# Kernel optimization log

Measured on AMD Instinct MI355X. Metric: run time of the kernel, lower is better.

## Reference

```python
import jax, jax.numpy as jnp
import numpy as np

N = 50000      # nodes
E = 800000     # edges
F_IN = 128     # input features
H = 64         # hidden channels
G = 64         # graphs in batch
EPS = 1e-5


def setup_inputs() -> dict:
    key = jax.random.key(0)
    ks = jax.random.split(key, 24)
    def nrm(k, s):
        return jax.random.normal(k, s, dtype=jnp.float32) * 0.05
    inp = {
        "x": nrm(ks[0], (N, F_IN)),
        "edge_index": jax.random.randint(ks[1], (2, E), 0, N),
        "batch": jnp.sort(jax.random.randint(ks[2], (N,), 0, G)),
        # GCNConv weights (stored [in, out]; math equivalent to torch Linear)
        "W0": nrm(ks[3], (F_IN, H)), "b0": nrm(ks[4], (H,)),
        "W1": nrm(ks[5], (H, H)),    "b1": nrm(ks[6], (H,)),
        "W2": nrm(ks[7], (H, H)),    "b2": nrm(ks[8], (H,)),
        # residual linears
        "RW0": nrm(ks[9], (F_IN, H)),  "rb0": nrm(ks[10], (H,)),
        "RW1": nrm(ks[11], (H, H)),    "rb1": nrm(ks[12], (H,)),
        "RW2": nrm(ks[13], (H, H)),    "rb2": nrm(ks[14], (H,)),
        # layernorm gamma/beta
        "g0": jnp.ones((H,), jnp.float32), "be0": jnp.zeros((H,), jnp.float32),
        "g1": jnp.ones((H,), jnp.float32), "be1": jnp.zeros((H,), jnp.float32),
        "g2": jnp.ones((H,), jnp.float32), "be2": jnp.zeros((H,), jnp.float32),
        # final readout linear
        "lw": nrm(ks[15], (H, 1)), "lb": nrm(ks[16], (1,)),
    }
    return inp


def _layernorm(x, g, b):
    mu = jnp.mean(x, axis=-1, keepdims=True)
    var = jnp.mean(jnp.square(x - mu), axis=-1, keepdims=True)
    return (x - mu) * jax.lax.rsqrt(var + EPS) * g + b


def reference(x, edge_index, batch,
              W0, b0, W1, b1, W2, b2,
              RW0, rb0, RW1, rb1, RW2, rb2,
              g0, be0, g1, be1, g2, be2,
              lw, lb):
    n = x.shape[0]
    loops = jnp.arange(n)
    row = jnp.concatenate([edge_index[0], loops])  # source
    col = jnp.concatenate([edge_index[1], loops])  # target
    # symmetric GCN normalization with self-loops (PyG gcn_norm)
    deg = jax.ops.segment_sum(jnp.ones_like(col, dtype=x.dtype), col, num_segments=n)
    dis = jnp.where(deg > 0, deg ** -0.5, 0.0)
    norm = dis[row] * dis[col]  # [E+N]

    params = [(W0, b0, RW0, rb0, g0, be0),
              (W1, b1, RW1, rb1, g1, be1),
              (W2, b2, RW2, rb2, g2, be2)]
    n_layers = len(params)
    for i, (W, b, RW, rb, g, be) in enumerate(params):
        h = x @ W                                                  # [n, H]
        agg = jax.ops.segment_sum(h[row] * norm[:, None], col, num_segments=n) + b
        x = agg + (x @ RW + rb)                                    # residual
        # dropout: eval mode -> identity
        x = _layernorm(x, g, be)
        if i < n_layers - 1:
            x = jax.nn.relu(x)

    # global mean pool over graphs
    counts = jax.ops.segment_sum(jnp.ones((n,), x.dtype), batch, num_segments=G)
    pooled = jax.ops.segment_sum(x, batch, num_segments=G) / jnp.maximum(counts, 1.0)[:, None]
    return pooled @ lw + lb  # [G, 1]
```

## Files before the change

### kernel.cpp

```cpp
#include <hip/hip_runtime.h>
#include <hip/hip_bf16.h>

#define HID 64
#define NGRAPH 64
#define BSH 7
#define NCH 384

static inline size_t align256(size_t x) { return (x + 255) & ~(size_t)255; }

typedef __attribute__((ext_vector_type(8))) short bf16x8;
typedef __attribute__((ext_vector_type(4))) float f32x4;

__device__ __forceinline__ float ldf(const void* p, size_t i, int f32) {
    if (f32) return ((const float*)p)[i];
    unsigned int w = ((unsigned int)((const unsigned short*)p)[i]) << 16;
    return __uint_as_float(w);
}
__device__ __forceinline__ float bf2f(unsigned short u) {
    return __uint_as_float(((unsigned int)u) << 16);
}
__device__ __forceinline__ unsigned short f2bf(float f) {
    __hip_bfloat16 h = __float2bfloat16(f);
    return *(unsigned short*)&h;
}

__device__ __forceinline__ unsigned char f2e4m3(float f) {
#if defined(__has_builtin) && __has_builtin(__builtin_amdgcn_cvt_pk_fp8_f32)
    int r = __builtin_amdgcn_cvt_pk_fp8_f32(f, f, 0, false);
    return (unsigned char)(r & 0xFF);
#else
    unsigned u = __float_as_uint(f);
    unsigned s = (u >> 24) & 0x80;
    unsigned a = u & 0x7FFFFFFF;
    float af = __uint_as_float(a);
    if (af < 0.015625f) {
        int m = (int)rintf(af * 512.f);
        return (unsigned char)(s | m);
    }
    unsigned r = a + 0x7FFFF + ((a >> 20) & 1);
    int e = (int)(r >> 23) - 127;
    if (e > 8) return (unsigned char)(s | 0x7E);
    return (unsigned char)(s | ((e + 7) << 3) | ((r >> 20) & 7));
#endif
}
template <int IDX>
__device__ __forceinline__ float d8(unsigned p) {
#if defined(__has_builtin) && __has_builtin(__builtin_amdgcn_cvt_f32_fp8)
    return __builtin_amdgcn_cvt_f32_fp8(p, IDX);
#else
    unsigned b = (p >> (IDX * 8)) & 0xFF;
    unsigned e = (b >> 3) & 0xF, m = b & 7;
    float v = e ? __uint_as_float(((e + 120) << 23) | (m << 20))
                : (float)m * (1.f / 512.f);
    return (b & 0x80) ? -v : v;
#endif
}

__global__ void k_sniff(const unsigned short* __restrict__ x, int nwords, int* __restrict__ flag,
                        float* __restrict__ gsum, int* __restrict__ gcnt) {
    __shared__ int cw, cz;
    int t = threadIdx.x;
    if (t == 0) { cw = 0; cz = 0; }
    if (t < NGRAPH) { gsum[t] = 0.f; gcnt[t] = 0; }
    __syncthreads();
    int weird = 0, evenzero = 0;
    for (int i = t; i < nwords; i += blockDim.x) {
        unsigned short u = x[i];
        int e = (u >> 7) & 0xFF;
        if (e >= 128) weird++;
        if (((i & 1) == 0) && ((u & 0x7FFF) == 0)) evenzero++;
    }
    atomicAdd(&cw, weird);
    atomicAdd(&cz, evenzero);
    __syncthreads();
    if (t == 0) *flag = (cw > nwords / 16 || cz > nwords / 8) ? 1 : 0;
}

__global__ __launch_bounds__(256) void k_prep(const int* __restrict__ batch, int* __restrict__ gcnt,
                                              int n, int nbG,
                                              const void* W0, const void* RW0, const void* b0, const void* rb0,
                                              const void* W1, const void* RW1, const void* b1, const void* rb1,
                                              const void* W2, const void* RW2, const void* b2, const void* rb2,
                                              const int* __restrict__ dflag,
                                              unsigned short* wt0, unsigned short* wt1, unsigned short* wt2,
                                              float* bcat,
                                              const int* __restrict__ ecol, int e, int nbuck,
                                              int* __restrict__ hist) {
    __shared__ int sh[1024];
    int b = blockIdx.x, t = threadIdx.x;
    if (b < nbG) {
        if (t < NGRAPH) sh[t] = 0;
        __syncthreads();
        int i = b * 256 + t;
        if (i < n) atomicAdd(&sh[batch[i]], 1);
        __syncthreads();
        if (t < NGRAPH && sh[t] > 0) atomicAdd(&gcnt[t], sh[t]);
    } else if (b < nbG + 130) {
        int f = *dflag;
        int i = (b - nbG) * 256 + t;
        if (i < 16384) {
            int nn = i >> 7, k = i & 127;
            float v = (nn < 64) ? ldf(W0, (size_t)k * 64 + nn, f) : ldf(RW0, (size_t)k * 64 + (nn - 64), f);
            wt0[nn * 128 + k] = f2bf(v);
        } else if (i < 24576) {
            int j = i - 16384; int nn = j >> 6, k = j & 63;
            float v = (nn < 64) ? ldf(W1, (size_t)k * 64 + nn, f) : ldf(RW1, (size_t)k * 64 + (nn - 64), f);
            wt1[nn * 64 + k] = f2bf(v);
        } else if (i < 32768) {
            int j = i - 24576; int nn = j >> 6, k = j & 63;
            float v = (nn < 64) ? ldf(W2, (size_t)k * 64 + nn, f) : ldf(RW2, (size_t)k * 64 + (nn - 64), f);
            wt2[nn * 64 + k] = f2bf(v);
        } else if (i < 32768 + 192) {
            int j = i - 32768; int l = j >> 6, c = j & 63;
            const void* bb = (l == 0) ? b0 : (l == 1) ? b1 : b2;
            const void* rr = (l == 0) ? rb0 : (l == 1) ? rb1 : rb2;
            bcat[l * 64 + c] = ldf(bb, c, f) + ldf(rr, c, f);
        }
    } else {
        int c = b - nbG - 130;
        for (int i = t; i < nbuck; i += 256) sh[i] = 0;
        __syncthreads();
        int per = (e + NCH - 1) / NCH;
        int s = c * per, en = min(e, s + per);
        for (int i = s + t; i < en; i += 256)
            atomicAdd(&sh[ecol[i] >> BSH], 1);
        __syncthreads();
        for (int i = t; i < nbuck; i += 256) hist[i * NCH + c] = sh[i];
    }
}

__global__ void k_scan1(const int* __restrict__ src, int* __restrict__ bsum, int n) {
    __shared__ int s[256];
    int t = threadIdx.x;
    int base = blockIdx.x * 1024 + t * 4;
    int sum = 0;
#pragma unroll
    for (int j = 0; j < 4; j++) { int i = base + j; if (i < n) sum += src[i]; }
    s[t] = sum;
    __syncthreads();
    for (int o = 128; o > 0; o >>= 1) {
        if (t < o) s[t] += s[t + o];
        __syncthreads();
    }
    if (t == 0) bsum[blockIdx.x] = s[0];
}

__global__ void k_scan2(const int* __restrict__ bsum, int* __restrict__ bscan,
                        int* __restrict__ out, int nb, int n) {
    __shared__ int s[256];
    int t = threadIdx.x;
    int v = (t < nb) ? bsum[t] : 0;
    s[t] = v;
    __syncthreads();
    for (int o = 1; o < 256; o <<= 1) {
        int x = (t >= o) ? s[t - o] : 0;
        __syncthreads();
        s[t] += x;
        __syncthreads();
    }
    if (t < nb) bscan[t] = s[t] - v;
    if (t == nb - 1) out[n] = s[t];
}

__global__ void k_scan3(const int* __restrict__ src, const int* __restrict__ bscan,
                        int* __restrict__ out, int n) {
    __shared__ int s[256];
    int t = threadIdx.x;
    int base = blockIdx.x * 1024 + t * 4;
    int tsum = 0;
#pragma unroll
    for (int j = 0; j < 4; j++) { int i = base + j; if (i < n) tsum += src[i]; }
    s[t] = tsum;
    __syncthreads();
    for (int o = 1; o < 256; o <<= 1) {
        int x = (t >= o) ? s[t - o] : 0;
        __syncthreads();
        s[t] += x;
        __syncthreads();
    }
    int off = bscan[blockIdx.x] + s[t] - tsum;
#pragma unroll
    for (int j = 0; j < 4; j++) {
        int i = base + j;
        if (i < n) { out[i] = off; off += src[i]; }
    }
}

__global__ __launch_bounds__(256) void k_scatter(const int* __restrict__ erow,
                                                 const int* __restrict__ ecol, int e, int nbuck,
                                                 const int* __restrict__ hoffs,
                                                 int* __restrict__ esrc,
                                                 unsigned char* __restrict__ et7) {
    __shared__ int cur[1024];
    int c = blockIdx.x, t = threadIdx.x;
    for (int i = t; i < nbuck; i += 256) cur[i] = hoffs[i * NCH + c];
    __syncthreads();
    int per = (e + NCH - 1) / NCH;
    int s = c * per, en = min(e, s + per);
    for (int i = s + t; i < en; i += 256) {
        int tg = ecol[i];
        int p = atomicAdd(&cur[tg >> BSH], 1);
        esrc[p] = erow[i];
        et7[p] = (unsigned char)(tg & 127);
    }
}

__global__ __launch_bounds__(256) void k_bucket(const int* __restrict__ esrc,
                                                const unsigned char* __restrict__ et7,
                                                const int* __restrict__ hoffs,
                                                int nbuck, int n, int e,
                                                int* __restrict__ offs, float* __restrict__ dis,
                                                int* __restrict__ csr) {
    __shared__ int hist[128];
    __shared__ int lofs[128];
    __shared__ int curs[128];
    int b = blockIdx.x, t = threadIdx.x;
    int nb0 = b << BSH;
    int nn = n - nb0; if (nn > 128) nn = 128;
    int s = hoffs[b * NCH];
    int en = (b + 1 < nbuck) ? hoffs[(b + 1) * NCH] : e;
    if (t < 128) hist[t] = 0;
    __syncthreads();
    for (int i = s + t; i < en; i += 256)
        atomicAdd(&hist[et7[i]], 1);
    __syncthreads();
    if (t < 128) lofs[t] = hist[t];
    __syncthreads();
    for (int o = 1; o < 128; o <<= 1) {
        int v = (t < 128 && t >= o) ? lofs[t - o] : 0;
        __syncthreads();
        if (t < 128) lofs[t] += v;
        __syncthreads();
    }
    if (t < nn) {
        int ex = s + lofs[t] - hist[t];
        offs[nb0 + t] = ex;
        curs[t] = ex;
        dis[nb0 + t] = rsqrtf((float)(hist[t] + 1));
    }
    if (b == nbuck - 1 && t == 0) offs[n] = e;
    __syncthreads();
    for (int i = s + t; i < en; i += 256) {
        int p = atomicAdd(&curs[et7[i]], 1);
        csr[p] = esrc[i];
    }
}

template <int K, bool XFLAG, bool LO>
__global__ __launch_bounds__(256) void k_gemm(const void* __restrict__ xin,
                                              const unsigned short* __restrict__ wt,
                                              const float* __restrict__ bcat,
                                              const float* __restrict__ dis,
                                              const int* __restrict__ dflag,
                                              unsigned char* __restrict__ hs,
                                              float* __restrict__ base, int n) {
    const int KP = K + 8;
    __shared__ unsigned short sXh[64 * KP];
    __shared__ unsigned short sXl[LO ? 64 * KP : 1];
    int f32 = *dflag;
    int tid = threadIdx.x;
    int row0 = blockIdx.x * 64;

    if (XFLAG && !f32) {
        const uint4* xv = (const uint4*)xin;
        const int C = K / 8;
        for (int i = tid; i < 64 * C; i += 256) {
            int r = i / C, c = i % C;
            int gr = row0 + r;
            uint4 v = (gr < n) ? xv[(size_t)gr * C + c] : make_uint4(0, 0, 0, 0);
            *(uint4*)&sXh[r * KP + c * 8] = v;
        }
    } else if (XFLAG) {
        for (int i = tid; i < 64 * K; i += 256) {
            int r = i / K, k = i - r * K;
            int gr = row0 + r;
            float v = (gr < n) ? ((const float*)xin)[(size_t)gr * K + k] : 0.f;
            sXh[r * KP + k] = f2bf(v);
        }
    } else {
        const float4* xv = (const float4*)xin;
        const int C = K / 4;
        for (int i = tid; i < 64 * C; i += 256) {
            int r = i / C, c = i % C;
            int gr = row0 + r;
            float4 v = (gr < n) ? xv[(size_t)gr * C + c] : make_float4(0.f, 0.f, 0.f, 0.f);
            ushort4 h, lo;
            h.x = f2bf(v.x); h.y = f2bf(v.y); h.z = f2bf(v.z); h.w = f2bf(v.w);
            if (LO) {
                lo.x = f2bf(v.x - bf2f(h.x)); lo.y = f2bf(v.y - bf2f(h.y));
                lo.z = f2bf(v.z - bf2f(h.z)); lo.w = f2bf(v.w - bf2f(h.w));
            }
            *(ushort4*)&sXh[r * KP + c * 4] = h;
            if (LO) *(ushort4*)&sXl[r * KP + c * 4] = lo;
        }
    }
    __syncthreads();

    int w = tid >> 6, lane = tid & 63;
    int m = lane & 15, q = lane >> 4;
    f32x4 acc[8];
#pragma unroll
    for (int ct = 0; ct < 8; ct++) acc[ct] = (f32x4){0.f, 0.f, 0.f, 0.f};

    int arow = w * 16 + m;
#pragma unroll 1
    for (int ks = 0; ks < K / 32; ks++) {
        int ka = ks * 32 + q * 8;
        bf16x8 ah = *(const bf16x8*)&sXh[arow * KP + ka];
        bf16x8 al;
        if (LO) al = *(const bf16x8*)&sXl[arow * KP + ka];
#pragma unroll
        for (int ct = 0; ct < 8; ct++) {
            bf16x8 bb = *(const bf16x8*)(wt + (size_t)(ct * 16 + m) * K + ka);
            acc[ct] = __builtin_amdgcn_mfma_f32_16x16x32_bf16(ah, bb, acc[ct], 0, 0, 0);
            if (LO) acc[ct] = __builtin_amdgcn_mfma_f32_16x16x32_bf16(al, bb, acc[ct], 0, 0, 0);
        }
    }

#pragma unroll
    for (int ct = 0; ct < 4; ct++) {
        int col = ct * 16 + m;
#pragma unroll
        for (int reg = 0; reg < 4; reg++) {
            int r = row0 + w * 16 + q * 4 + reg;
            if (r < n) {
                float dv = dis[r];
                float h = acc[ct][reg] * dv;
                hs[(size_t)r * 64 + col] = f2e4m3(h);
                base[(size_t)r * 64 + col] = h * dv + acc[ct + 4][reg] + bcat[col];
            }
        }
    }
}

template <bool FINAL>
__global__ __launch_bounds__(1024) void k_agg_ln(const unsigned char* __restrict__ hs,
                                                 const float* __restrict__ base,
                                                 const float* __restrict__ dis,
                                                 const int* __restrict__ offs,
                                                 const int* __restrict__ csr,
                                                 const void* __restrict__ gam,
                                                 const void* __restrict__ bet,
                                                 const int* __restrict__ dflag,
                                                 float* __restrict__ xout, int n, int relu,
                                                 const int* __restrict__ batch,
                                                 const void* __restrict__ lw,
                                                 float* __restrict__ gsum) {
    __shared__ float sG[FINAL ? NGRAPH : 1];
    int f32 = *dflag;
    int t = threadIdx.x;
    if (FINAL) {
        if (t < NGRAPH) sG[t] = 0.f;
        __syncthreads();
    }
    int grp = t >> 4;
    int l = t & 15;
    int gl0 = (t & 63) & ~15;
    int v = blockIdx.x * 64 + grp;
    if (v < n) {
        int s = offs[v];
        int e2 = offs[v + 1];
        float4 bv = *(const float4*)&base[(size_t)v * 64 + l * 4];
        float dv = dis[v];
        float a0 = 0.f, a1 = 0.f, a2 = 0.f, a3 = 0.f;
        int myidx = (s + l < e2) ? csr[s + l] : 0;
        for (int gbase = s; gbase < e2; gbase += 16) {
            int cnt = e2 - gbase; if (cnt > 16) cnt = 16;
            int cur = myidx;
            int nxt = gbase + 16;
            if (nxt < e2) myidx = (nxt + l < e2) ? csr[nxt + l] : 0;
            int j = 0;
            for (; j + 7 < cnt; j += 8) {
                int s0 = __shfl(cur, gl0 + j, 64);
                int s1 = __shfl(cur, gl0 + j + 1, 64);
                int s2 = __shfl(cur, gl0 + j + 2, 64);
                int s3 = __shfl(cur, gl0 + j + 3, 64);
                int s4 = __shfl(cur, gl0 + j + 4, 64);
                int s5 = __shfl(cur, gl0 + j + 5, 64);
                int s6 = __shfl(cur, gl0 + j + 6, 64);
                int s7 = __shfl(cur, gl0 + j + 7, 64);
                unsigned p0 = *(const unsigned*)(hs + (size_t)s0 * 64 + l * 4);
                unsigned p1 = *(const unsigned*)(hs + (size_t)s1 * 64 + l * 4);
                unsigned p2 = *(const unsigned*)(hs + (size_t)s2 * 64 + l * 4);
                unsigned p3 = *(const unsigned*)(hs + (size_t)s3 * 64 + l * 4);
                unsigned p4 = *(const unsigned*)(hs + (size_t)s4 * 64 + l * 4);
                unsigned p5 = *(const unsigned*)(hs + (size_t)s5 * 64 + l * 4);
                unsigned p6 = *(const unsigned*)(hs + (size_t)s6 * 64 + l * 4);
                unsigned p7 = *(const unsigned*)(hs + (size_t)s7 * 64 + l * 4);
                a0 += ((d8<0>(p0) + d8<0>(p1)) + (d8<0>(p2) + d8<0>(p3)))
                    + ((d8<0>(p4) + d8<0>(p5)) + (d8<0>(p6) + d8<0>(p7)));
                a1 += ((d8<1>(p0) + d8<1>(p1)) + (d8<1>(p2) + d8<1>(p3)))
                    + ((d8<1>(p4) + d8<1>(p5)) + (d8<1>(p6) + d8<1>(p7)));
                a2 += ((d8<2>(p0) + d8<2>(p1)) + (d8<2>(p2) + d8<2>(p3)))
                    + ((d8<2>(p4) + d8<2>(p5)) + (d8<2>(p6) + d8<2>(p7)));
                a3 += ((d8<3>(p0) + d8<3>(p1)) + (d8<3>(p2) + d8<3>(p3)))
                    + ((d8<3>(p4) + d8<3>(p5)) + (d8<3>(p6) + d8<3>(p7)));
            }
            for (; j + 3 < cnt; j += 4) {
                int s0 = __shfl(cur, gl0 + j, 64);
                int s1 = __shfl(cur, gl0 + j + 1, 64);
                int s2 = __shfl(cur, gl0 + j + 2, 64);
                int s3 = __shfl(cur, gl0 + j + 3, 64);
                unsigned p0 = *(const unsigned*)(hs + (size_t)s0 * 64 + l * 4);
                unsigned p1 = *(const unsigned*)(hs + (size_t)s1 * 64 + l * 4);
                unsigned p2 = *(const unsigned*)(hs + (size_t)s2 * 64 + l * 4);
                unsigned p3 = *(const unsigned*)(hs + (size_t)s3 * 64 + l * 4);
                a0 += (d8<0>(p0) + d8<0>(p1)) + (d8<0>(p2) + d8<0>(p3));
                a1 += (d8<1>(p0) + d8<1>(p1)) + (d8<1>(p2) + d8<1>(p3));
                a2 += (d8<2>(p0) + d8<2>(p1)) + (d8<2>(p2) + d8<2>(p3));
                a3 += (d8<3>(p0) + d8<3>(p1)) + (d8<3>(p2) + d8<3>(p3));
            }
            for (; j < cnt; j++) {
                int s0 = __shfl(cur, gl0 + j, 64);
                unsigned p0 = *(const unsigned*)(hs + (size_t)s0 * 64 + l * 4);
                a0 += d8<0>(p0);
                a1 += d8<1>(p0);
                a2 += d8<2>(p0);
                a3 += d8<3>(p0);
            }
        }
        a0 = bv.x + dv * a0;
        a1 = bv.y + dv * a1;
        a2 = bv.z + dv * a2;
        a3 = bv.w + dv * a3;
        float m = a0 + a1 + a2 + a3;
        m += __shfl_xor(m, 1, 64); m += __shfl_xor(m, 2, 64);
        m += __shfl_xor(m, 4, 64); m += __shfl_xor(m, 8, 64);
        m *= (1.f / 64.f);
        float d0 = a0 - m, d1 = a1 - m, d2 = a2 - m, d3 = a3 - m;
        float var = d0 * d0 + d1 * d1 + d2 * d2 + d3 * d3;
        var += __shfl_xor(var, 1, 64); var += __shfl_xor(var, 2, 64);
        var += __shfl_xor(var, 4, 64); var += __shfl_xor(var, 8, 64);
        var *= (1.f / 64.f);
        float rs = rsqrtf(var + 1e-5f);
        float y0 = d0 * rs * ldf(gam, l * 4 + 0, f32) + ldf(bet, l * 4 + 0, f32);
        float y1 = d1 * rs * ldf(gam, l * 4 + 1, f32) + ldf(bet, l * 4 + 1, f32);
        float y2 = d2 * rs * ldf(gam, l * 4 + 2, f32) + ldf(bet, l * 4 + 2, f32);
        float y3 = d3 * rs * ldf(gam, l * 4 + 3, f32) + ldf(bet, l * 4 + 3, f32);
        if (relu) {
            y0 = fmaxf(y0, 0.f); y1 = fmaxf(y1, 0.f);
            y2 = fmaxf(y2, 0.f); y3 = fmaxf(y3, 0.f);
        }
        if (!FINAL) {
            *(float4*)&xout[(size_t)v * 64 + l * 4] = make_float4(y0, y1, y2, y3);
        } else {
            float val = y0 * ldf(lw, l * 4 + 0, f32) + y1 * ldf(lw, l * 4 + 1, f32)
                      + y2 * ldf(lw, l * 4 + 2, f32) + y3 * ldf(lw, l * 4 + 3, f32);
            val += __shfl_xor(val, 1, 64); val += __shfl_xor(val, 2, 64);
            val += __shfl_xor(val, 4, 64); val += __shfl_xor(val, 8, 64);
            if (l == 0) atomicAdd(&sG[batch[v]], val);
        }
    }
    if (FINAL) {
        __syncthreads();
        if (t < NGRAPH && sG[t] != 0.f) atomicAdd(&gsum[t], sG[t]);
    }
}

__global__ void k_final(const float* __restrict__ gsum, const int* __restrict__ gcnt,
                        const void* __restrict__ lb, const int* __restrict__ dflag,
                        void* __restrict__ out, int g) {
    int f32 = *dflag;
    int i = threadIdx.x;
    if (i < g) {
        float c = fmaxf((float)gcnt[i], 1.f);
        float v = gsum[i] / c + ldf(lb, 0, f32);
        if (f32) ((float*)out)[i] = v;
        else ((__hip_bfloat16*)out)[i] = __float2bfloat16(v);
    }
}

extern "C" void kernel_launch(void* const* d_in, const int* in_sizes, int n_in,
                              void* d_out, int out_size, void* d_ws, size_t ws_size,
                              hipStream_t stream) {
    const void* x_in = d_in[0];
    const int* edge_index = (const int*)d_in[1];
    const int* batch = (const int*)d_in[2];
    const void *W0 = d_in[3], *b0 = d_in[4], *W1 = d_in[5], *b1 = d_in[6],
               *W2 = d_in[7], *b2 = d_in[8];
    const void *RW0 = d_in[9], *rb0 = d_in[10], *RW1 = d_in[11], *rb1 = d_in[12],
               *RW2 = d_in[13], *rb2 = d_in[14];
    const void *g0 = d_in[15], *be0 = d_in[16], *g1 = d_in[17], *be1 = d_in[18],
               *g2 = d_in[19], *be2 = d_in[20], *lw = d_in[21], *lb = d_in[22];

    const int N = in_sizes[2];
    const int E = in_sizes[1] / 2;
    const int* erow = edge_index;
    const int* ecol = edge_index + E;
    const int nbuck = (N + 127) >> BSH;
    const int T = nbuck * NCH;

    char* p = (char*)d_ws;
    size_t off = 0;
    float* dis = (float*)(p + off);  off = align256(off + (size_t)N * 4);
    int* offs = (int*)(p + off);     off = align256(off + (size_t)(N + 1) * 4);
    int* csr = (int*)(p + off);      off = align256(off + (size_t)E * 4);
    int* esrc = (int*)(p + off);     off = align256(off + (size_t)E * 4);
    unsigned char* et7 = (unsigned char*)(p + off); off = align256(off + (size_t)E);
    int* hist = (int*)(p + off);     off = align256(off + (size_t)T * 4);
    int* hoffs = (int*)(p + off);    off = align256(off + (size_t)(T + 1) * 4);
    unsigned char* hs = (unsigned char*)(p + off); off = align256(off + (size_t)N * HID);
    float* base = (float*)(p + off); off = align256(off + (size_t)N * HID * 4);
    float* xbuf = (float*)(p + off); off = align256(off + (size_t)N * HID * 4);
    unsigned short* wt0 = (unsigned short*)(p + off); off = align256(off + 16384 * 2);
    unsigned short* wt1 = (unsigned short*)(p + off); off = align256(off + 8192 * 2);
    unsigned short* wt2 = (unsigned short*)(p + off); off = align256(off + 8192 * 2);
    float* bcat = (float*)(p + off); off = align256(off + 192 * 4);
    int* bsum = (int*)(p + off);     off = align256(off + 256 * 4);
    int* bscan = (int*)(p + off);    off = align256(off + 256 * 4);
    float* gsum = (float*)(p + off); off = align256(off + NGRAPH * 4);
    int* gcnt = (int*)(p + off);     off = align256(off + NGRAPH * 4);
    int* dflag = (int*)(p + off);    off = align256(off + 4);
    (void)ws_size;

    const int TB = 256;
    int nbG = (N + TB - 1) / TB;
    int nbT = (T + 1023) / 1024;
    int nb_gemm = (N + 63) / 64;
    int nb_agg = (N + 63) / 64;

    k_sniff<<<1, 256, 0, stream>>>((const unsigned short*)x_in, 8192, dflag, gsum, gcnt);
    k_prep<<<nbG + 130 + NCH, TB, 0, stream>>>(batch, gcnt, N, nbG,
                                               W0, RW0, b0, rb0, W1, RW1, b1, rb1,
                                               W2, RW2, b2, rb2, dflag, wt0, wt1, wt2, bcat,
                                               ecol, E, nbuck, hist);
    k_scan1<<<nbT, TB, 0, stream>>>(hist, bsum, T);
    k_scan2<<<1, TB, 0, stream>>>(bsum, bscan, hoffs, nbT, T);
    k_scan3<<<nbT, TB, 0, stream>>>(hist, bscan, hoffs, T);
    k_scatter<<<NCH, TB, 0, stream>>>(erow, ecol, E, nbuck, hoffs, esrc, et7);
    k_bucket<<<nbuck, TB, 0, stream>>>(esrc, et7, hoffs, nbuck, N, E, offs, dis, csr);

    k_gemm<128, true, false><<<nb_gemm, TB, 0, stream>>>(x_in, wt0, bcat, dis, dflag, hs, base, N);
    k_agg_ln<false><<<nb_agg, 1024, 0, stream>>>(hs, base, dis, offs, csr, g0, be0, dflag,
                                                 xbuf, N, 1, nullptr, nullptr, nullptr);
    k_gemm<64, false, true><<<nb_gemm, TB, 0, stream>>>(xbuf, wt1, bcat + 64, dis, dflag, hs, base, N);
    k_agg_ln<false><<<nb_agg, 1024, 0, stream>>>(hs, base, dis, offs, csr, g1, be1, dflag,
                                                 xbuf, N, 1, nullptr, nullptr, nullptr);
    k_gemm<64, false, true><<<nb_gemm, TB, 0, stream>>>(xbuf, wt2, bcat + 128, dis, dflag, hs, base, N);
    k_agg_ln<true><<<nb_agg, 1024, 0, stream>>>(hs, base, dis, offs, csr, g2, be2, dflag,
                                                nullptr, N, 0, batch, lw, gsum);

    k_final<<<1, 64, 0, stream>>>(gsum, gcnt, lb, dflag, d_out, NGRAPH);
}
```

Measured before the change: 295.7 us.

## Issue 16 gathers at once in aggregation, widen scatter blocks, unroll GEMM K loop

The aggregation inner loop now issues all 16 neighbour gathers of a full chunk before accumulating, and drops the software prefetch of the next chunk's CSR indices in favour of loading them per chunk. The scatter kernel moves from 256 to 512 threads per block, and the GEMM K loop is fully unrolled. The aim is more memory-level parallelism in the gather-bound aggregation and less loop overhead, at the cost of more registers and a lost index prefetch. Summation order also changes slightly.

```diff
diff --git a/kernel.cpp b/kernel.cpp
--- a/kernel.cpp
+++ b/kernel.cpp
@@ -186,18 +186,18 @@
     }
 }
 
-__global__ __launch_bounds__(256) void k_scatter(const int* __restrict__ erow,
+__global__ __launch_bounds__(512) void k_scatter(const int* __restrict__ erow,
                                                  const int* __restrict__ ecol, int e, int nbuck,
                                                  const int* __restrict__ hoffs,
                                                  int* __restrict__ esrc,
                                                  unsigned char* __restrict__ et7) {
     __shared__ int cur[1024];
     int c = blockIdx.x, t = threadIdx.x;
-    for (int i = t; i < nbuck; i += 256) cur[i] = hoffs[i * NCH + c];
+    for (int i = t; i < nbuck; i += 512) cur[i] = hoffs[i * NCH + c];
     __syncthreads();
     int per = (e + NCH - 1) / NCH;
     int s = c * per, en = min(e, s + per);
-    for (int i = s + t; i < en; i += 256) {
+    for (int i = s + t; i < en; i += 512) {
         int tg = ecol[i];
         int p = atomicAdd(&cur[tg >> BSH], 1);
         esrc[p] = erow[i];
@@ -303,7 +303,7 @@
     for (int ct = 0; ct < 8; ct++) acc[ct] = (f32x4){0.f, 0.f, 0.f, 0.f};
 
     int arow = w * 16 + m;
-#pragma unroll 1
+#pragma unroll
     for (int ks = 0; ks < K / 32; ks++) {
         int ka = ks * 32 + q * 8;
         bf16x8 ah = *(const bf16x8*)&sXh[arow * KP + ka];
@@ -363,60 +363,63 @@
         float4 bv = *(const float4*)&base[(size_t)v * 64 + l * 4];
         float dv = dis[v];
         float a0 = 0.f, a1 = 0.f, a2 = 0.f, a3 = 0.f;
-        int myidx = (s + l < e2) ? csr[s + l] : 0;
         for (int gbase = s; gbase < e2; gbase += 16) {
             int cnt = e2 - gbase; if (cnt > 16) cnt = 16;
-            int cur = myidx;
-            int nxt = gbase + 16;
-            if (nxt < e2) myidx = (nxt + l < e2) ? csr[nxt + l] : 0;
-            int j = 0;
-            for (; j + 7 < cnt; j += 8) {
-                int s0 = __shfl(cur, gl0 + j, 64);
-                int s1 = __shfl(cur, gl0 + j + 1, 64);
-                int s2 = __shfl(cur, gl0 + j + 2, 64);
-                int s3 = __shfl(cur, gl0 + j + 3, 64);
-                int s4 = __shfl(cur, gl0 + j + 4, 64);
-                int s5 = __shfl(cur, gl0 + j + 5, 64);
-                int s6 = __shfl(cur, gl0 + j + 6, 64);
-                int s7 = __shfl(cur, gl0 + j + 7, 64);
-                unsigned p0 = *(const unsigned*)(hs + (size_t)s0 * 64 + l * 4);
-                unsigned p1 = *(const unsigned*)(hs + (size_t)s1 * 64 + l * 4);
-                unsigned p2 = *(const unsigned*)(hs + (size_t)s2 * 64 + l * 4);
-                unsigned p3 = *(const unsigned*)(hs + (size_t)s3 * 64 + l * 4);
-                unsigned p4 = *(const unsigned*)(hs + (size_t)s4 * 64 + l * 4);
-                unsigned p5 = *(const unsigned*)(hs + (size_t)s5 * 64 + l * 4);
-                unsigned p6 = *(const unsigned*)(hs + (size_t)s6 * 64 + l * 4);
-                unsigned p7 = *(const unsigned*)(hs + (size_t)s7 * 64 + l * 4);
-                a0 += ((d8<0>(p0) + d8<0>(p1)) + (d8<0>(p2) + d8<0>(p3)))
-                    + ((d8<0>(p4) + d8<0>(p5)) + (d8<0>(p6) + d8<0>(p7)));
-                a1 += ((d8<1>(p0) + d8<1>(p1)) + (d8<1>(p2) + d8<1>(p3)))
-                    + ((d8<1>(p4) + d8<1>(p5)) + (d8<1>(p6) + d8<1>(p7)));
-                a2 += ((d8<2>(p0) + d8<2>(p1)) + (d8<2>(p2) + d8<2>(p3)))
-                    + ((d8<2>(p4) + d8<2>(p5)) + (d8<2>(p6) + d8<2>(p7)));
-                a3 += ((d8<3>(p0) + d8<3>(p1)) + (d8<3>(p2) + d8<3>(p3)))
-                    + ((d8<3>(p4) + d8<3>(p5)) + (d8<3>(p6) + d8<3>(p7)));
-            }
-            for (; j + 3 < cnt; j += 4) {
-                int s0 = __shfl(cur, gl0 + j, 64);
-                int s1 = __shfl(cur, gl0 + j + 1, 64);
-                int s2 = __shfl(cur, gl0 + j + 2, 64);
-                int s3 = __shfl(cur, gl0 + j + 3, 64);
-                unsigned p0 = *(const unsigned*)(hs + (size_t)s0 * 64 + l * 4);
-                unsigned p1 = *(const unsigned*)(hs + (size_t)s1 * 64 + l * 4);
-                unsigned p2 = *(const unsigned*)(hs + (size_t)s2 * 64 + l * 4);
-                unsigned p3 = *(const unsigned*)(hs + (size_t)s3 * 64 + l * 4);
-                a0 += (d8<0>(p0) + d8<0>(p1)) + (d8<0>(p2) + d8<0>(p3));
-                a1 += (d8<1>(p0) + d8<1>(p1)) + (d8<1>(p2) + d8<1>(p3));
-                a2 += (d8<2>(p0) + d8<2>(p1)) + (d8<2>(p2) + d8<2>(p3));
-                a3 += (d8<3>(p0) + d8<3>(p1)) + (d8<3>(p2) + d8<3>(p3));
-            }
-            for (; j < cnt; j++) {
-                int s0 = __shfl(cur, gl0 + j, 64);
-                unsigned p0 = *(const unsigned*)(hs + (size_t)s0 * 64 + l * 4);
-                a0 += d8<0>(p0);
-                a1 += d8<1>(p0);
-                a2 += d8<2>(p0);
-                a3 += d8<3>(p0);
+            int cur = (gbase + l < e2) ? csr[gbase + l] : 0;
+            if (cnt == 16) {
+                unsigned pp[16];
+#pragma unroll
+                for (int j = 0; j < 16; j++) {
+                    int sj = __shfl(cur, gl0 + j, 64);
+                    pp[j] = *(const unsigned*)(hs + (size_t)sj * 64 + l * 4);
+                }
+#pragma unroll
+                for (int j = 0; j < 16; j++) {
+                    a0 += d8<0>(pp[j]);
+                    a1 += d8<1>(pp[j]);
+                    a2 += d8<2>(pp[j]);
+                    a3 += d8<3>(pp[j]);
+                }
+            } else {
+                int j = 0;
+                for (; j + 7 < cnt; j += 8) {
+                    unsigned pp[8];
+#pragma unroll
+                    for (int u = 0; u < 8; u++) {
+                        int sj = __shfl(cur, gl0 + j + u, 64);
+                        pp[u] = *(const unsigned*)(hs + (size_t)sj * 64 + l * 4);
+                    }
+#pragma unroll
+                    for (int u = 0; u < 8; u++) {
+                        a0 += d8<0>(pp[u]);
+                        a1 += d8<1>(pp[u]);
+                        a2 += d8<2>(pp[u]);
+                        a3 += d8<3>(pp[u]);
+                    }
+                }
+                for (; j + 3 < cnt; j += 4) {
+                    unsigned pp[4];
+#pragma unroll
+                    for (int u = 0; u < 4; u++) {
+                        int sj = __shfl(cur, gl0 + j + u, 64);
+                        pp[u] = *(const unsigned*)(hs + (size_t)sj * 64 + l * 4);
+                    }
+#pragma unroll
+                    for (int u = 0; u < 4; u++) {
+                        a0 += d8<0>(pp[u]);
+                        a1 += d8<1>(pp[u]);
+                        a2 += d8<2>(pp[u]);
+                        a3 += d8<3>(pp[u]);
+                    }
+                }
+                for (; j < cnt; j++) {
+                    int sj = __shfl(cur, gl0 + j, 64);
+                    unsigned p0 = *(const unsigned*)(hs + (size_t)sj * 64 + l * 4);
+                    a0 += d8<0>(p0);
+                    a1 += d8<1>(p0);
+                    a2 += d8<2>(p0);
+                    a3 += d8<3>(p0);
+                }
             }
         }
         a0 = bv.x + dv * a0;
@@ -527,7 +530,7 @@
     k_scan1<<<nbT, TB, 0, stream>>>(hist, bsum, T);
     k_scan2<<<1, TB, 0, stream>>>(bsum, bscan, hoffs, nbT, T);
     k_scan3<<<nbT, TB, 0, stream>>>(hist, bscan, hoffs, T);
-    k_scatter<<<NCH, TB, 0, stream>>>(erow, ecol, E, nbuck, hoffs, esrc, et7);
+    k_scatter<<<NCH, 512, 0, stream>>>(erow, ecol, E, nbuck, hoffs, esrc, et7);
     k_bucket<<<nbuck, TB, 0, stream>>>(esrc, et7, hoffs, nbuck, N, E, offs, dis, csr);
 
     k_gemm<128, true, false><<<nb_gemm, TB, 0, stream>>>(x_in, wt0, bcat, dis, dflag, hs, base, N);
```

Result: slower. 305.8 us (+3.4%).
